# Optimization experiments

Hardware: AMD Instinct MI355X
Metric: run time of the kernel (lower is better)

The kernel has to match this reference:

```python
import jax, jax.numpy as jnp
import numpy as np
from jax import lax

SHIFT_SIZE = 5
PAD = SHIFT_SIZE // 2


def _shift(xn, axis):
    """xn: (B, C, Hp, Wp, Dp) zero-padded volume. Split channels into
    SHIFT_SIZE chunks and roll each chunk by shift in [-PAD, PAD] along `axis`."""
    chunks = jnp.split(xn, SHIFT_SIZE, axis=1)
    shifted = [jnp.roll(c, s, axis=axis) for c, s in zip(chunks, range(-PAD, PAD + 1))]
    return jnp.concatenate(shifted, axis=1)


def _shift_tokens(x, H, W, D, axis):
    """x: (B, N, C) tokens -> shifted tokens (B, N, C). axis=2 shifts H, axis=3 shifts W."""
    B, N, C = x.shape
    xn = x.transpose(0, 2, 1).reshape(B, C, H, W, D)
    xn = jnp.pad(xn, ((0, 0), (0, 0), (PAD, PAD), (PAD, PAD), (PAD, PAD)))
    xs = _shift(xn, axis)
    xs = xs[:, :, PAD:PAD + H, PAD:PAD + W, PAD:PAD + D]
    return xs.reshape(B, C, N).transpose(0, 2, 1)


def setup_inputs() -> dict:
    key = jax.random.key(0)
    ks = jax.random.split(key, 4)
    B, H, W, D = 2, 32, 32, 32
    N = H * W * D
    Cin, Ch = 160, 640
    return {
        "x": jax.random.normal(ks[0], (B, N, Cin), jnp.float32),
        "fc1_w": jax.random.normal(ks[1], (Ch, Cin), jnp.float32) * 0.02,
        "fc1_b": jnp.zeros((Ch,), jnp.float32),
        "dw_w": jax.random.normal(ks[2], (Ch, 1, 3, 3, 3), jnp.float32) * (2.0 / 27.0) ** 0.5,
        "dw_b": jnp.zeros((Ch,), jnp.float32),
        "fc2_w": jax.random.normal(ks[3], (Cin, Ch), jnp.float32) * 0.02,
        "fc2_b": jnp.zeros((Cin,), jnp.float32),
        "H": H, "W": W, "D": D,
    }


def reference(x, fc1_w, fc1_b, dw_w, dw_b, fc2_w, fc2_b, H, W, D):
    B, N, Cin = x.shape
    Ch = fc1_w.shape[0]
    # shift block 1: roll along H (axis 2)
    xs = _shift_tokens(x, H, W, D, axis=2)
    # fc1
    h = jnp.einsum('bnc,hc->bnh', xs, fc1_w) + fc1_b  # (B, N, Ch)
    # depthwise 3x3x3 conv
    hv = h.transpose(0, 2, 1).reshape(B, Ch, H, W, D)
    hv = lax.conv_general_dilated(
        hv, dw_w, window_strides=(1, 1, 1), padding='SAME',
        feature_group_count=Ch,
        dimension_numbers=('NCDHW', 'OIDHW', 'NCDHW'))
    hv = hv + dw_b[None, :, None, None, None]
    hv = jax.nn.gelu(hv, approximate=False)
    h = hv.reshape(B, Ch, N).transpose(0, 2, 1)
    # shift block 2: roll along W (axis 3)
    hs = _shift_tokens(h, H, W, D, axis=3)
    # fc2
    out = jnp.einsum('bnh,oh->bno', hs, fc2_w) + fc2_b  # (B, N, Cin)
    return out
```

## Files before the change

kernel.cpp:

```cpp
#include <hip/hip_runtime.h>
#include <hip/hip_bf16.h>
#include <math.h>

#define DEVI __device__ __forceinline__

typedef _Float16 f16;
typedef f16 f16x2 __attribute__((ext_vector_type(2)));
typedef f16 f16x4 __attribute__((ext_vector_type(4)));
typedef f16 f16x8 __attribute__((ext_vector_type(8)));
typedef float f32x4 __attribute__((ext_vector_type(4)));

constexpr int Bb = 2, Hh = 32, Ww = 32, Dd = 32;
constexpr int Nn = Hh * Ww * Dd;
constexpr int BN = Bb * Nn;
constexpr int CIN = 160, CHH = 640;
constexpr int PD = 34;
constexpr int PT = PD * PD * PD;

constexpr size_t W1_OFF  = 0;
constexpr size_t W2_OFF  = W1_OFF + (size_t)CHH * CIN * 2;
constexpr size_t WTH_OFF = W2_OFF + (size_t)CIN * CHH * 2;
constexpr size_t ZP_OFF  = WTH_OFF + 34816;
constexpr size_t U_OFF   = 458752;
constexpr size_t H1P_OFF = U_OFF + (size_t)BN * CHH * 2;

DEVI void async16(const void* g, void* l) {
  __builtin_amdgcn_global_load_lds(
      (const __attribute__((address_space(1))) void*)g,
      (__attribute__((address_space(3))) void*)l, 16, 0, 0);
}

constexpr int PREPW_BLOCKS = 876;
constexpr int ZPAD_BLOCKS  = (2 * PT * 80 + 255) / 256;

__global__ __launch_bounds__(256) void k_prep(const float* __restrict__ fc1w,
                                              const float* __restrict__ fc2w,
                                              const float* __restrict__ dww,
                                              f16* __restrict__ w1h,
                                              f16* __restrict__ w2h,
                                              f16* __restrict__ wTh,
                                              unsigned* __restrict__ zp,
                                              f16* __restrict__ h1p) {
  const int bid = blockIdx.x;
  const int tid = threadIdx.x;
  if (bid < PREPW_BLOCKS) {
    int i = bid * 256 + tid;
    const int NW = CHH * CIN;
    if (i < NW) {
      w1h[i] = (f16)fc1w[i];
    } else if (i < 2 * NW) {
      w2h[i - NW] = (f16)fc2w[i - NW];
    } else if (i < 2 * NW + 27 * CHH) {
      int j = i - 2 * NW;
      int ch = j / 27, tap = j % 27;
      wTh[tap * CHH + ch] = (f16)dww[j];
    } else if (i < 2 * NW + 27 * CHH + 2048) {
      zp[i - (2 * NW + 27 * CHH)] = 0u;
    }
    return;
  }
  int g = (bid - PREPW_BLOCKS) * 256 + tid;
  int p = g / 80;
  int c = g - p * 80;
  if (p >= 2 * PT) return;
  int r = p % PT;
  int hp = r / (PD * PD);
  int r2 = r % (PD * PD);
  int wp = r2 / PD, dp = r2 % PD;
  bool pad = (hp == 0) | (hp == PD - 1) | (wp == 0) | (wp == PD - 1) |
             (dp == 0) | (dp == PD - 1);
  if (!pad) return;
  f16x8 z = {};
  *(f16x8*)&h1p[(size_t)p * CHH + c * 8] = z;
}

__global__ __launch_bounds__(256) void k_gemm1(const float* __restrict__ x,
                                               const f16* __restrict__ w1h,
                                               const float* __restrict__ fc1b,
                                               f16* __restrict__ h1p) {
  constexpr int LDA = 168;
  __shared__ f16 lsA[128 * LDA];
  __shared__ f16 lsB[128 * 32];
  const int tid = threadIdx.x;
  const int lane = tid & 63, wave = tid >> 6;
  const int row0 = blockIdx.x * 128;
  const int wr = wave >> 1, wc = wave & 1;
  const int rl = lane & 15, kb = (lane >> 4) * 8;

#pragma unroll
  for (int i = 0; i < 20; ++i) {
    int c = i * 256 + tid;
    int row = c / 40;
    int q = c - row * 40;
    int ch0 = q * 4;
    int ks = ch0 >> 5;
    int s = ks - 2;
    int t = row0 + row;
    int h = (t >> 10) & 31;
    int hs = h - s;
    float4 v = {0.f, 0.f, 0.f, 0.f};
    if (hs >= 0 && hs < 32)
      v = *(const float4*)&x[(long)(t - s * 1024) * CIN + ch0];
    f16x4 o4;
    o4[0] = (f16)v.x; o4[1] = (f16)v.y; o4[2] = (f16)v.z; o4[3] = (f16)v.w;
    *(f16x4*)&lsA[row * LDA + ch0] = o4;
  }
  __syncthreads();

  for (int nt = 0; nt < 5; ++nt) {
    const int col0 = nt * 128;
    f32x4 acc[4][4] = {};
    for (int ks = 0; ks < 5; ++ks) {
#pragma unroll
      for (int issue = 0; issue < 2; ++issue) {
        int c = issue * 256 + tid;
        int br = c >> 2;
        int ju = (c & 3) ^ (br & 3);
        const f16* src = w1h + (size_t)(col0 + br) * CIN + ks * 32 + ju * 8;
        async16(src, (char*)lsB + issue * 4096 + wave * 1024);
      }
      __syncthreads();
      f16x8 af[4], bfr[4];
#pragma unroll
      for (int mi = 0; mi < 4; ++mi)
        af[mi] = *(const f16x8*)&lsA[(wr * 64 + mi * 16 + rl) * LDA + ks * 32 + kb];
#pragma unroll
      for (int ni = 0; ni < 4; ++ni) {
        int row = wc * 64 + ni * 16 + rl;
        int u = (lane >> 4) ^ (rl & 3);
        bfr[ni] = *(const f16x8*)&lsB[row * 32 + u * 8];
      }
#pragma unroll
      for (int mi = 0; mi < 4; ++mi)
#pragma unroll
        for (int ni = 0; ni < 4; ++ni)
          acc[mi][ni] = __builtin_amdgcn_mfma_f32_16x16x32_f16(af[mi], bfr[ni], acc[mi][ni], 0, 0, 0);
      __syncthreads();
    }
    const int rq = lane >> 4;
#pragma unroll
    for (int mi = 0; mi < 4; ++mi) {
      int rowq = row0 + wr * 64 + mi * 16 + rq * 4;
      int bq = rowq >> 15;
      int nq = rowq & 32767;
      int hq = nq >> 10, wq = (nq >> 5) & 31, dq = nq & 31;
      size_t pos = (size_t)((bq * PD + hq + 1) * PD + (wq + 1)) * PD + (dq + 1);
      f16* dst0 = h1p + pos * CHH;
#pragma unroll
      for (int ni = 0; ni < 4; ++ni) {
        int col = col0 + wc * 64 + ni * 16 + rl;
        float bias = fc1b[col];
#pragma unroll
        for (int r = 0; r < 4; ++r)
          dst0[(size_t)r * CHH + col] = (f16)(acc[mi][ni][r] + bias);
      }
    }
  }
}

__global__ __launch_bounds__(256) void k_conv(const f16* __restrict__ h1p,
                                              const f16* __restrict__ wTh,
                                              const float* __restrict__ dwb,
                                              f16* __restrict__ h2h) {
  __shared__ f16 lw[27 * 64];
  __shared__ f16 lb[64];
  const int tid = threadIdx.x;
  const int bid = blockIdx.x;
  const int wg = (bid & 7) * 640 + (bid >> 3);
  const int cg = wg % 10;
  const int quad = wg / 10;
#pragma unroll
  for (int i = 0; i < 7; ++i) {
    int idx = i * 256 + tid;
    if (idx < 27 * 64) lw[idx] = wTh[(idx >> 6) * CHH + cg * 64 + (idx & 63)];
  }
  if (tid < 64) lb[tid] = (f16)dwb[cg * 64 + tid];
  __syncthreads();

  const int lane = tid & 63, wave = tid >> 6;
  const int line = quad * 4 + wave;
  const int c8 = lane & 7, dq = lane >> 3;
  const int d0 = dq * 4;
  const int ch0 = cg * 64 + c8 * 8;
  const int w = line & 31, h = (line >> 5) & 31, b = line >> 10;

  const size_t cidx = (size_t)((b * PD + h) * PD + w) * PD + d0;
  const f16* base = h1p + cidx * CHH + ch0;

  f16x8 acc[4];
  {
    f16x8 binit = *(const f16x8*)&lb[c8 * 8];
    acc[0] = binit; acc[1] = binit; acc[2] = binit; acc[3] = binit;
  }

#pragma unroll
  for (int kz = 0; kz < 3; ++kz) {
#pragma unroll
    for (int ky = 0; ky < 3; ++ky) {
      const f16* pb = base + (size_t)(kz * PD + ky) * PD * CHH;
      f16x8 wt[3];
#pragma unroll
      for (int kx = 0; kx < 3; ++kx)
        wt[kx] = *(const f16x8*)&lw[((kz * 9 + ky * 3 + kx) << 6) + c8 * 8];
      f16x8 v[6];
#pragma unroll
      for (int j = 0; j < 6; ++j)
        v[j] = *(const f16x8*)(pb + (size_t)j * CHH);
#pragma unroll
      for (int o = 0; o < 4; ++o)
#pragma unroll
        for (int kx = 0; kx < 3; ++kx)
          acc[o] = v[o + kx] * wt[kx] + acc[o];
    }
  }

  const ptrdiff_t obase = (ptrdiff_t)(line * 32 + d0) * CHH + ch0;
#pragma unroll
  for (int o = 0; o < 4; ++o) {
    f16x8 xa = acc[o];
    f16x8 ov;
#pragma unroll
    for (int j = 0; j < 8; j += 2) {
      float g01[2];
#pragma unroll
      for (int u2 = 0; u2 < 2; ++u2) {
        float xv = (float)xa[j + u2];
        float x2 = xv * xv;
        float uu = xv * (2.3022078f + 0.102943324f * x2);
        float e = __builtin_exp2f(uu);
        float r = __builtin_amdgcn_rcpf(1.0f + e);
        g01[u2] = xv - xv * r;
      }
      f16x2 pk = __builtin_bit_cast(f16x2, __builtin_amdgcn_cvt_pkrtz(g01[0], g01[1]));
      ov[j] = pk[0]; ov[j + 1] = pk[1];
    }
    *(f16x8*)&h2h[obase + (ptrdiff_t)o * CHH] = ov;
  }
}

__global__ __launch_bounds__(256) void k_gemm2(const f16* __restrict__ h2h,
                                               const f16* __restrict__ w2h,
                                               const float* __restrict__ fc2b,
                                               const f16* __restrict__ zp,
                                               float* __restrict__ out) {
  __shared__ f16 lsA[128 * 64];
  __shared__ f16 lsB[160 * 64];
  const int tid = threadIdx.x, lane = tid & 63, wave = tid >> 6;
  const int row0 = blockIdx.x * 128;
  const int rl = lane & 15;

  f32x4 acc[2][10] = {};

  for (int kt = 0; kt < 10; ++kt) {
    __syncthreads();
    const int k0 = kt * 64;
    const int s = (kt >> 1) - 2;
#pragma unroll
    for (int issue = 0; issue < 4; ++issue) {
      int c = issue * 256 + tid;
      int ar = c >> 3;
      int ju = (c & 7) ^ (ar & 7);
      int kc = ju * 8;
      int t = row0 + ar;
      int w = (t >> 5) & 31;
      int wsv = w - s;
      const f16* src;
      if (wsv >= 0 && wsv < 32)
        src = h2h + (size_t)(t - s * 32) * CHH + k0 + kc;
      else
        src = zp + (size_t)(c & 63) * 8;
      async16(src, (char*)lsA + issue * 4096 + wave * 1024);
    }
#pragma unroll
    for (int issue = 0; issue < 5; ++issue) {
      int c = issue * 256 + tid;
      int br = c >> 3;
      int ju = (c & 7) ^ (br & 7);
      const f16* src = w2h + (size_t)br * CHH + k0 + ju * 8;
      async16(src, (char*)lsB + issue * 4096 + wave * 1024);
    }
    __syncthreads();
#pragma unroll
    for (int kk = 0; kk < 2; ++kk) {
      f16x8 af[2], bfr[10];
#pragma unroll
      for (int mi = 0; mi < 2; ++mi) {
        int row = wave * 32 + mi * 16 + rl;
        int u = (kk * 4 + (lane >> 4)) ^ (rl & 7);
        af[mi] = *(const f16x8*)&lsA[row * 64 + u * 8];
      }
#pragma unroll
      for (int ni = 0; ni < 10; ++ni) {
        int row = ni * 16 + rl;
        int u = (kk * 4 + (lane >> 4)) ^ (rl & 7);
        bfr[ni] = *(const f16x8*)&lsB[row * 64 + u * 8];
      }
#pragma unroll
      for (int mi = 0; mi < 2; ++mi)
#pragma unroll
        for (int ni = 0; ni < 10; ++ni)
          acc[mi][ni] = __builtin_amdgcn_mfma_f32_16x16x32_f16(af[mi], bfr[ni], acc[mi][ni], 0, 0, 0);
    }
  }
  const int rq = lane >> 4;
#pragma unroll
  for (int mi = 0; mi < 2; ++mi) {
#pragma unroll
    for (int ni = 0; ni < 10; ++ni) {
      int col = ni * 16 + rl;
      float bias = fc2b[col];
#pragma unroll
      for (int r = 0; r < 4; ++r) {
        int row = row0 + wave * 32 + mi * 16 + rq * 4 + r;
        out[(size_t)row * CIN + col] = acc[mi][ni][r] + bias;
      }
    }
  }
}

extern "C" void kernel_launch(void* const* d_in, const int* in_sizes, int n_in,
                              void* d_out, int out_size, void* d_ws, size_t ws_size,
                              hipStream_t stream) {
  const float* x    = (const float*)d_in[0];
  const float* fc1w = (const float*)d_in[1];
  const float* fc1b = (const float*)d_in[2];
  const float* dww  = (const float*)d_in[3];
  const float* dwb  = (const float*)d_in[4];
  const float* fc2w = (const float*)d_in[5];
  const float* fc2b = (const float*)d_in[6];

  char* ws = (char*)d_ws;
  f16* w1h  = (f16*)(ws + W1_OFF);
  f16* w2h  = (f16*)(ws + W2_OFF);
  f16* wTh  = (f16*)(ws + WTH_OFF);
  f16* zp   = (f16*)(ws + ZP_OFF);
  f16* h2h  = (f16*)(ws + U_OFF);
  f16* h1p  = (f16*)(ws + H1P_OFF);
  float* out = (float*)d_out;

  k_prep<<<PREPW_BLOCKS + ZPAD_BLOCKS, 256, 0, stream>>>(
      fc1w, fc2w, dww, w1h, w2h, wTh, (unsigned*)zp, h1p);
  k_gemm1<<<512, 256, 0, stream>>>(x, w1h, fc1b, h1p);
  k_conv<<<5120, 256, 0, stream>>>(h1p, wTh, dwb, h2h);
  k_gemm2<<<512, 256, 0, stream>>>(h2h, w2h, fc2b, zp, out);
}
```

Before: 131.0 us.

## Compute two adjacent W-lines per wave in depthwise conv and use packed half GELU

```diff
diff --git a/kernel.cpp b/kernel.cpp
--- a/kernel.cpp
+++ b/kernel.cpp
@@ -1,5 +1,6 @@
 #include <hip/hip_runtime.h>
 #include <hip/hip_bf16.h>
+#include <hip/hip_fp16.h>
 #include <math.h>
 
 #define DEVI __device__ __forceinline__
@@ -28,6 +29,26 @@
   __builtin_amdgcn_global_load_lds(
       (const __attribute__((address_space(1))) void*)g,
       (__attribute__((address_space(3))) void*)l, 16, 0, 0);
+}
+
+DEVI f16x8 gelu8(f16x8 xa) {
+  const __half2 C1 = __float2half2_rn(2.3022078f);
+  const __half2 C2 = __float2half2_rn(0.102943324f);
+  const __half2 ONE = __float2half2_rn(1.0f);
+  f16x8 out;
+#pragma unroll
+  for (int j = 0; j < 8; j += 2) {
+    __half2 xv = __builtin_bit_cast(__half2, f16x2{xa[j], xa[j + 1]});
+    __half2 x2 = __hmul2(xv, xv);
+    __half2 t  = __hfma2(x2, C2, C1);
+    __half2 u  = __hmul2(xv, t);
+    __half2 e  = h2exp2(u);
+    __half2 r  = h2rcp(__hadd2(e, ONE));
+    __half2 g  = __hsub2(xv, __hmul2(xv, r));
+    f16x2 gg = __builtin_bit_cast(f16x2, g);
+    out[j] = gg[0]; out[j + 1] = gg[1];
+  }
+  return out;
 }
 
 constexpr int PREPW_BLOCKS = 876;
@@ -166,9 +187,9 @@
   __shared__ f16 lb[64];
   const int tid = threadIdx.x;
   const int bid = blockIdx.x;
-  const int wg = (bid & 7) * 640 + (bid >> 3);
+  const int wg = (bid & 7) * 320 + (bid >> 3);
   const int cg = wg % 10;
-  const int quad = wg / 10;
+  const int oct = wg / 10;
 #pragma unroll
   for (int i = 0; i < 7; ++i) {
     int idx = i * 256 + tid;
@@ -178,63 +199,60 @@
   __syncthreads();
 
   const int lane = tid & 63, wave = tid >> 6;
-  const int line = quad * 4 + wave;
+  const int L0 = oct * 8 + wave * 2;
   const int c8 = lane & 7, dq = lane >> 3;
   const int d0 = dq * 4;
   const int ch0 = cg * 64 + c8 * 8;
-  const int w = line & 31, h = (line >> 5) & 31, b = line >> 10;
-
-  const size_t cidx = (size_t)((b * PD + h) * PD + w) * PD + d0;
+  const int w0 = L0 & 31, h = (L0 >> 5) & 31, b = L0 >> 10;
+
+  const size_t cidx = (size_t)((b * PD + h) * PD + w0) * PD + d0;
   const f16* base = h1p + cidx * CHH + ch0;
 
-  f16x8 acc[4];
+  f16x8 acc0[4], acc1[4];
   {
     f16x8 binit = *(const f16x8*)&lb[c8 * 8];
-    acc[0] = binit; acc[1] = binit; acc[2] = binit; acc[3] = binit;
+#pragma unroll
+    for (int o = 0; o < 4; ++o) { acc0[o] = binit; acc1[o] = binit; }
   }
 
 #pragma unroll
   for (int kz = 0; kz < 3; ++kz) {
-#pragma unroll
-    for (int ky = 0; ky < 3; ++ky) {
-      const f16* pb = base + (size_t)(kz * PD + ky) * PD * CHH;
-      f16x8 wt[3];
+    f16x8 wt[3][3];
+#pragma unroll
+    for (int ky = 0; ky < 3; ++ky)
 #pragma unroll
       for (int kx = 0; kx < 3; ++kx)
-        wt[kx] = *(const f16x8*)&lw[((kz * 9 + ky * 3 + kx) << 6) + c8 * 8];
+        wt[ky][kx] = *(const f16x8*)&lw[((kz * 9 + ky * 3 + kx) << 6) + c8 * 8];
+#pragma unroll
+    for (int py = 0; py < 4; ++py) {
+      const f16* pb = base + (size_t)(kz * PD + py) * PD * CHH;
       f16x8 v[6];
 #pragma unroll
       for (int j = 0; j < 6; ++j)
         v[j] = *(const f16x8*)(pb + (size_t)j * CHH);
-#pragma unroll
-      for (int o = 0; o < 4; ++o)
-#pragma unroll
-        for (int kx = 0; kx < 3; ++kx)
-          acc[o] = v[o + kx] * wt[kx] + acc[o];
-    }
-  }
-
-  const ptrdiff_t obase = (ptrdiff_t)(line * 32 + d0) * CHH + ch0;
+      if (py < 3) {
+#pragma unroll
+        for (int o = 0; o < 4; ++o)
+#pragma unroll
+          for (int kx = 0; kx < 3; ++kx)
+            acc0[o] = v[o + kx] * wt[py][kx] + acc0[o];
+      }
+      if (py >= 1) {
+#pragma unroll
+        for (int o = 0; o < 4; ++o)
+#pragma unroll
+          for (int kx = 0; kx < 3; ++kx)
+            acc1[o] = v[o + kx] * wt[py - 1][kx] + acc1[o];
+      }
+    }
+  }
+
+  const ptrdiff_t ob0 = (ptrdiff_t)(L0 * 32 + d0) * CHH + ch0;
+  const ptrdiff_t ob1 = ob0 + (ptrdiff_t)32 * CHH;
 #pragma unroll
   for (int o = 0; o < 4; ++o) {
-    f16x8 xa = acc[o];
-    f16x8 ov;
-#pragma unroll
-    for (int j = 0; j < 8; j += 2) {
-      float g01[2];
-#pragma unroll
-      for (int u2 = 0; u2 < 2; ++u2) {
-        float xv = (float)xa[j + u2];
-        float x2 = xv * xv;
-        float uu = xv * (2.3022078f + 0.102943324f * x2);
-        float e = __builtin_exp2f(uu);
-        float r = __builtin_amdgcn_rcpf(1.0f + e);
-        g01[u2] = xv - xv * r;
-      }
-      f16x2 pk = __builtin_bit_cast(f16x2, __builtin_amdgcn_cvt_pkrtz(g01[0], g01[1]));
-      ov[j] = pk[0]; ov[j + 1] = pk[1];
-    }
-    *(f16x8*)&h2h[obase + (ptrdiff_t)o * CHH] = ov;
+    *(f16x8*)&h2h[ob0 + (ptrdiff_t)o * CHH] = gelu8(acc0[o]);
+    *(f16x8*)&h2h[ob1 + (ptrdiff_t)o * CHH] = gelu8(acc1[o]);
   }
 }
 
@@ -341,6 +359,6 @@
   k_prep<<<PREPW_BLOCKS + ZPAD_BLOCKS, 256, 0, stream>>>(
       fc1w, fc2w, dww, w1h, w2h, wTh, (unsigned*)zp, h1p);
   k_gemm1<<<512, 256, 0, stream>>>(x, w1h, fc1b, h1p);
-  k_conv<<<5120, 256, 0, stream>>>(h1p, wTh, dwb, h2h);
+  k_conv<<<2560, 256, 0, stream>>>(h1p, wTh, dwb, h2h);
   k_gemm2<<<512, 256, 0, stream>>>(h2h, w2h, fc2b, zp, out);
 }
```

Measured after the change: 122.9 us. -6.1%, faster.
